# Kernel optimization log

Measured on AMD Instinct MI355X. Metric: run time of the kernel, lower is better.

## Reference

```python
import jax, jax.numpy as jnp
import numpy as np

B, G, D, H, KD = 32, 512, 128, 4, 32  # batch, graph, embed_dim, n_heads, key_dim=embed//heads
NORM = 1.0 / np.sqrt(KD).astype(np.float32)  # MultiHeadCompat norm_factor = 1/sqrt(key_dim)


def _uniform(k, shape, fan):
    s = 1.0 / np.sqrt(fan).astype(np.float32)
    return jax.random.uniform(k, shape, jnp.float32, -s, s)


def setup_inputs() -> dict:
    key = jax.random.key(0)
    ks = jax.random.split(key, 16)
    inp = {
        "h": jax.random.normal(ks[0], (B, G, D), jnp.float32),
        "pos_pickup": jax.random.randint(ks[1], (B,), 0, G),
        "pos_delivery": jax.random.randint(ks[2], (B,), 0, G),
        "rec": jax.random.randint(ks[3], (B, G), 0, G),
        # compater_insert1 / compater_insert2 projections: (n_heads, input_dim, key_dim)
        "Wq1": _uniform(ks[4], (H, D, KD), KD),
        "Wk1": _uniform(ks[5], (H, D, KD), KD),
        "Wq2": _uniform(ks[6], (H, D, KD), KD),
        "Wk2": _uniform(ks[7], (H, D, KD), KD),
        # agg MLP(16, 32, 32, 1); stored as (in, out) so y = x @ W + b
        "fc1_w": _uniform(ks[8], (16, 32), 16),
        "fc1_b": _uniform(ks[9], (32,), 32),
        "fc2_w": _uniform(ks[10], (32, 32), 32),
        "fc2_b": _uniform(ks[11], (32,), 32),
        "fc3_w": _uniform(ks[12], (32, 1), 32),
        "fc3_b": _uniform(ks[13], (1,), 1),
    }
    return inp


def _compat(qv, hh, Wq, Wk):
    # qv: (B, D) single query node; hh: (B, G, D)
    Q = jnp.einsum('bd,hdk->bhk', qv, Wq)       # (B, H, K)
    K = jnp.einsum('bgd,hdk->bhgk', hh, Wk)     # (B, H, G, K)
    return NORM * jnp.einsum('bhk,bhgk->bgh', Q, K)  # (B, G, H)


def reference(h, pos_pickup, pos_delivery, rec, Wq1, Wk1, Wq2, Wk2,
              fc1_w, fc1_b, fc2_w, fc2_b, fc3_w, fc3_b):
    b, g, d = h.shape
    ar = jnp.arange(b)
    h_pickup = h[ar, pos_pickup]      # (B, D)
    h_delivery = h[ar, pos_delivery]  # (B, D)
    h_neighbour = jnp.take_along_axis(h, rec[:, :, None], axis=1)  # (B, G, D)

    shp = (b, g, g, 4)
    c_pp = jnp.broadcast_to(_compat(h_pickup, h, Wq1, Wk1)[:, :, None, :], shp)
    c_po = jnp.broadcast_to(_compat(h_pickup, h_neighbour, Wq2, Wk2)[:, :, None, :], shp)
    c_dp = jnp.broadcast_to(_compat(h_delivery, h, Wq1, Wk1)[:, None, :, :], shp)
    c_do = jnp.broadcast_to(_compat(h_delivery, h_neighbour, Wq2, Wk2)[:, None, :, :], shp)
    x = jnp.concatenate([c_pp, c_po, c_dp, c_do], axis=-1)  # (B, G, G, 16)

    # agg MLP (dropout p=0.05 is identity at inference)
    x = jax.nn.relu(x @ fc1_w + fc1_b)
    x = jax.nn.relu(x @ fc2_w + fc2_b)
    return (x @ fc3_w + fc3_b)[..., 0]  # (B, G, G)
```

## Files before the change

kernel.cpp:

```cpp
#include <hip/hip_runtime.h>


#define B 32
#define G 512
#define D 128
#define NH 4
#define KD 32
#define NORMF 0.17677669529663687f

#define WS_P16H 131072
#define WS_Q16H 655360

typedef float v16f __attribute__((ext_vector_type(16)));
typedef _Float16 v8h __attribute__((ext_vector_type(8)));
typedef _Float16 h2v __attribute__((ext_vector_type(2)));

struct HQ { h2v h[4]; };

__device__ __forceinline__ v8h relu_add(const HQ& p, const HQ& q) {
  const h2v z = {(_Float16)0.0f, (_Float16)0.0f};
  HQ r;
#pragma unroll
  for (int i = 0; i < 4; ++i)
    r.h[i] = __builtin_elementwise_max(p.h[i] + q.h[i], z);
  return __builtin_bit_cast(v8h, r);
}

__global__ __launch_bounds__(256) void stage01(
    const float* __restrict__ h, const int* __restrict__ pp,
    const int* __restrict__ pd, const int* __restrict__ rec,
    const float* __restrict__ Wq1, const float* __restrict__ Wk1,
    const float* __restrict__ Wq2, const float* __restrict__ Wk2,
    const float* __restrict__ fc1_w, const float* __restrict__ fc1_b,
    float* __restrict__ ws) {
  const int bx = blockIdx.x;
  const int b = bx >> 3, g0 = (bx & 7) * 64;
  const int t = threadIdx.x;

  __shared__ float hp[D], hd[D];
  __shared__ float qq[4][NH * KD];
  __shared__ float sA[4][NH][D];
  __shared__ float sc[64][17];
  __shared__ float sout[64][33];

  if (t < 128) {
    hp[t] = h[((size_t)b * G + pp[b]) * D + t];
  } else {
    const int u = t - 128;
    hd[u] = h[((size_t)b * G + pd[b]) * D + u];
  }
  __syncthreads();

  if (t < 128) {
    const int hh = t >> 5, k = t & 31;
    const float* wq1 = Wq1 + hh * D * KD + k;
    const float* wq2 = Wq2 + hh * D * KD + k;
    float s1p = 0.f, s2p = 0.f, s1d = 0.f, s2d = 0.f;
    for (int d = 0; d < D; ++d) {
      const float w1 = wq1[d * KD], w2 = wq2[d * KD];
      const float xp = hp[d], xd = hd[d];
      s1p = fmaf(xp, w1, s1p);
      s2p = fmaf(xp, w2, s2p);
      s1d = fmaf(xd, w1, s1d);
      s2d = fmaf(xd, w2, s2d);
    }
    qq[0][t] = s1p; qq[1][t] = s2p; qq[2][t] = s1d; qq[3][t] = s2d;
  }
  __syncthreads();

  {
    const int d = t & 127;
    const int h0 = (t >> 7) * 2;
#pragma unroll
    for (int hh = h0; hh < h0 + 2; ++hh) {
      const float* wk1 = Wk1 + hh * D * KD + d * KD;
      const float* wk2 = Wk2 + hh * D * KD + d * KD;
      float apq = 0.f, apo = 0.f, adp = 0.f, ado = 0.f;
#pragma unroll
      for (int k = 0; k < KD; ++k) {
        const float w1 = wk1[k], w2 = wk2[k];
        apq = fmaf(qq[0][hh * 32 + k], w1, apq);
        adp = fmaf(qq[2][hh * 32 + k], w1, adp);
        apo = fmaf(qq[1][hh * 32 + k], w2, apo);
        ado = fmaf(qq[3][hh * 32 + k], w2, ado);
      }
      sA[0][hh][d] = NORMF * apq;
      sA[1][hh][d] = NORMF * apo;
      sA[2][hh][d] = NORMF * adp;
      sA[3][hh][d] = NORMF * ado;
    }
  }
  __syncthreads();

  const int gl = t & 63;
  const int hh = __builtin_amdgcn_readfirstlane(t >> 6);
  const int g = g0 + gl;
  const float4* hg4 = (const float4*)(h + ((size_t)b * G + g) * D);
  const float4* hn4 = (const float4*)(h + ((size_t)b * G + rec[b * G + g]) * D);

  float cpp = 0.f, cpo = 0.f, cdp = 0.f, cdo = 0.f;
#pragma unroll 4
  for (int d4 = 0; d4 < 32; ++d4) {
    const float4 x = hg4[d4], y = hn4[d4];
    const float4 a1 = *(const float4*)&sA[0][hh][4 * d4];
    const float4 a2 = *(const float4*)&sA[1][hh][4 * d4];
    const float4 a3 = *(const float4*)&sA[2][hh][4 * d4];
    const float4 a4 = *(const float4*)&sA[3][hh][4 * d4];
    cpp = fmaf(x.x, a1.x, fmaf(x.y, a1.y, fmaf(x.z, a1.z, fmaf(x.w, a1.w, cpp))));
    cpo = fmaf(y.x, a2.x, fmaf(y.y, a2.y, fmaf(y.z, a2.z, fmaf(y.w, a2.w, cpo))));
    cdp = fmaf(x.x, a3.x, fmaf(x.y, a3.y, fmaf(x.z, a3.z, fmaf(x.w, a3.w, cdp))));
    cdo = fmaf(y.x, a4.x, fmaf(y.y, a4.y, fmaf(y.z, a4.z, fmaf(y.w, a4.w, cdo))));
  }
  sc[gl][hh] = cpp; sc[gl][4 + hh] = cpo; sc[gl][8 + hh] = cdp; sc[gl][12 + hh] = cdo;
  __syncthreads();

  float u[16];
#pragma unroll
  for (int i = 0; i < 16; ++i) u[i] = sc[gl][i];

  float pv[8], qv[8];
#pragma unroll
  for (int jj = 0; jj < 8; ++jj) {
    const int j = hh * 8 + jj;
    float p = 0.f, q = fc1_b[j];
#pragma unroll
    for (int i = 0; i < 8; ++i) {
      p = fmaf(u[i], fc1_w[i * 32 + j], p);
      q = fmaf(u[8 + i], fc1_w[(8 + i) * 32 + j], q);
    }
    pv[jj] = p; qv[jj] = q;
  }

#pragma unroll
  for (int jj = 0; jj < 8; ++jj) sout[gl][hh * 8 + jj] = pv[jj];
  __syncthreads();
  {
    unsigned* dst = (unsigned*)((unsigned short*)ws + WS_P16H) +
                    ((size_t)b * G + g0) * 16;
#pragma unroll
    for (int i = t; i < 1024; i += 256) {
      const int row = i >> 4, c0 = (2 * i) & 31;
      __fp16 __attribute__((ext_vector_type(2))) pk =
          __builtin_amdgcn_cvt_pkrtz(sout[row][c0], sout[row][c0 + 1]);
      dst[i] = *(const unsigned*)&pk;
    }
  }
  __syncthreads();
#pragma unroll
  for (int jj = 0; jj < 8; ++jj) sout[gl][hh * 8 + jj] = qv[jj];
  __syncthreads();
  {
    unsigned* dst = (unsigned*)((unsigned short*)ws + WS_Q16H) +
                    ((size_t)b * G + g0) * 16;
#pragma unroll
    for (int i = t; i < 1024; i += 256) {
      const int row = i >> 4, c0 = (2 * i) & 31;
      __fp16 __attribute__((ext_vector_type(2))) pk =
          __builtin_amdgcn_cvt_pkrtz(sout[row][c0], sout[row][c0 + 1]);
      dst[i] = *(const unsigned*)&pk;
    }
  }
}

__global__ __launch_bounds__(256) void mlp_pairs(
    const float* __restrict__ ws,
    const float* __restrict__ fc2_w, const float* __restrict__ fc2_b,
    const float* __restrict__ fc3_w, const float* __restrict__ fc3_b,
    float* __restrict__ out) {
  const int b = blockIdx.z;
  const int g1_0 = blockIdx.y * 16;
  const int g2_0 = blockIdx.x * 128;
  const int t = threadIdx.x;
  const int w = t >> 6, l = t & 63;
  const int col = l & 31;
  const int half = l >> 5;
  const int kb = half * 8;

  __shared__ __align__(16) unsigned short sPh[16 * 32];
  {
    const unsigned* Psrc = (const unsigned*)((const unsigned short*)ws + WS_P16H) +
                           ((size_t)b * G + g1_0) * 16;
    ((unsigned*)sPh)[t] = Psrc[t];
  }

  v8h A0, A1;
#pragma unroll
  for (int j = 0; j < 8; ++j) {
    A0[j] = (_Float16)fc2_w[(kb + j) * 32 + col];
    A1[j] = (_Float16)fc2_w[(16 + kb + j) * 32 + col];
  }
  v16f biasC;
  float w3v[16];
#pragma unroll
  for (int r = 0; r < 16; ++r) {
    const int n = (r & 3) + 8 * (r >> 2) + 4 * half;
    biasC[r] = fc2_b[n];
    w3v[r]   = fc3_w[n];
  }
  const float b3 = fc3_b[0];

  HQ qlo, qhi;
  {
    const unsigned short* qp = (const unsigned short*)ws + WS_Q16H +
        ((size_t)b * G + g2_0 + w * 32 + col) * 32;
    qlo = __builtin_bit_cast(HQ, *(const uint4*)(qp + kb));
    qhi = __builtin_bit_cast(HQ, *(const uint4*)(qp + 16 + kb));
  }
  __syncthreads();

  float* op = out + (((size_t)b * G + g1_0 + half) * G) + g2_0 + w * 32 + col;
#pragma unroll
  for (int i = 0; i < 8; ++i) {
    const int ra = 2 * i, rb = 2 * i + 1;
    const HQ palo = __builtin_bit_cast(HQ, *(const uint4*)(sPh + ra * 32 + kb));
    const HQ pahi = __builtin_bit_cast(HQ, *(const uint4*)(sPh + ra * 32 + 16 + kb));
    const HQ pblo = __builtin_bit_cast(HQ, *(const uint4*)(sPh + rb * 32 + kb));
    const HQ pbhi = __builtin_bit_cast(HQ, *(const uint4*)(sPh + rb * 32 + 16 + kb));

    const v8h Balo = relu_add(palo, qlo);
    const v8h Bahi = relu_add(pahi, qhi);
    const v8h Bblo = relu_add(pblo, qlo);
    const v8h Bbhi = relu_add(pbhi, qhi);

    v16f acca = __builtin_amdgcn_mfma_f32_32x32x16_f16(A0, Balo, biasC, 0, 0, 0);
    v16f accb = __builtin_amdgcn_mfma_f32_32x32x16_f16(A0, Bblo, biasC, 0, 0, 0);
    acca = __builtin_amdgcn_mfma_f32_32x32x16_f16(A1, Bahi, acca, 0, 0, 0);
    accb = __builtin_amdgcn_mfma_f32_32x32x16_f16(A1, Bbhi, accb, 0, 0, 0);

    float a0 = 0.f, a1 = 0.f, b0 = 0.f, b1 = 0.f;
#pragma unroll
    for (int r = 0; r < 16; r += 2) {
      a0 = fmaf(fmaxf(acca[r], 0.f), w3v[r], a0);
      a1 = fmaf(fmaxf(acca[r + 1], 0.f), w3v[r + 1], a1);
      b0 = fmaf(fmaxf(accb[r], 0.f), w3v[r], b0);
      b1 = fmaf(fmaxf(accb[r + 1], 0.f), w3v[r + 1], b1);
    }
    float sa = a0 + a1, sb = b0 + b1;
    sa += __shfl_xor(sa, 32);
    sb += __shfl_xor(sb, 32);
    op[(size_t)ra * G] = (half ? sb : sa) + b3;
  }
}

extern "C" void kernel_launch(void* const* d_in, const int* in_sizes, int n_in,
                              void* d_out, int out_size, void* d_ws, size_t ws_size,
                              hipStream_t stream) {
  const float* h     = (const float*)d_in[0];
  const int*   pp    = (const int*)d_in[1];
  const int*   pd    = (const int*)d_in[2];
  const int*   rec   = (const int*)d_in[3];
  const float* Wq1   = (const float*)d_in[4];
  const float* Wk1   = (const float*)d_in[5];
  const float* Wq2   = (const float*)d_in[6];
  const float* Wk2   = (const float*)d_in[7];
  const float* fc1_w = (const float*)d_in[8];
  const float* fc1_b = (const float*)d_in[9];
  const float* fc2_w = (const float*)d_in[10];
  const float* fc2_b = (const float*)d_in[11];
  const float* fc3_w = (const float*)d_in[12];
  const float* fc3_b = (const float*)d_in[13];
  float* out = (float*)d_out;
  float* ws  = (float*)d_ws;

  stage01<<<dim3(256), dim3(256), 0, stream>>>(
      h, pp, pd, rec, Wq1, Wk1, Wq2, Wk2, fc1_w, fc1_b, ws);
  mlp_pairs<<<dim3(4, 32, 32), dim3(256), 0, stream>>>(
      ws, fc2_w, fc2_b, fc3_w, fc3_b, out);
}
```

Baseline: 148.9 us.

## Double g2 tile per block, reuse P rows across two Q columns, pack epilogue

Each wave now covers two 32-wide g2 column groups against all 16 g1 rows, where before it covered one group against row pairs. Each P row loaded from shared memory feeds two MFMA chains, and the grid shrinks by half in x. The layer-3 epilogue uses packed float2 max/fma, and a single cross-half shuffle replaces two. The aim is fewer LDS reads, fewer shuffles and less VALU per output, at the cost of more registers per thread and fewer blocks.

```diff
diff --git a/kernel.cpp b/kernel.cpp
--- a/kernel.cpp
+++ b/kernel.cpp
@@ -12,10 +12,12 @@
 #define WS_Q16H 655360
 
 typedef float v16f __attribute__((ext_vector_type(16)));
+typedef float f2v __attribute__((ext_vector_type(2)));
 typedef _Float16 v8h __attribute__((ext_vector_type(8)));
 typedef _Float16 h2v __attribute__((ext_vector_type(2)));
 
 struct HQ { h2v h[4]; };
+struct F2x8 { f2v v[8]; };
 
 __device__ __forceinline__ v8h relu_add(const HQ& p, const HQ& q) {
   const h2v z = {(_Float16)0.0f, (_Float16)0.0f};
@@ -169,7 +171,7 @@
     float* __restrict__ out) {
   const int b = blockIdx.z;
   const int g1_0 = blockIdx.y * 16;
-  const int g2_0 = blockIdx.x * 128;
+  const int g2_0 = blockIdx.x * 256;
   const int t = threadIdx.x;
   const int w = t >> 6, l = t & 63;
   const int col = l & 31;
@@ -190,55 +192,57 @@
     A1[j] = (_Float16)fc2_w[(16 + kb + j) * 32 + col];
   }
   v16f biasC;
-  float w3v[16];
+  F2x8 w3p;
 #pragma unroll
   for (int r = 0; r < 16; ++r) {
     const int n = (r & 3) + 8 * (r >> 2) + 4 * half;
     biasC[r] = fc2_b[n];
-    w3v[r]   = fc3_w[n];
+    ((float*)&w3p)[r] = fc3_w[n];
   }
   const float b3 = fc3_b[0];
 
-  HQ qlo, qhi;
-  {
+  HQ qlo[2], qhi[2];
+#pragma unroll
+  for (int c = 0; c < 2; ++c) {
     const unsigned short* qp = (const unsigned short*)ws + WS_Q16H +
-        ((size_t)b * G + g2_0 + w * 32 + col) * 32;
-    qlo = __builtin_bit_cast(HQ, *(const uint4*)(qp + kb));
-    qhi = __builtin_bit_cast(HQ, *(const uint4*)(qp + 16 + kb));
-  }
-  __syncthreads();
-
-  float* op = out + (((size_t)b * G + g1_0 + half) * G) + g2_0 + w * 32 + col;
-#pragma unroll
-  for (int i = 0; i < 8; ++i) {
-    const int ra = 2 * i, rb = 2 * i + 1;
-    const HQ palo = __builtin_bit_cast(HQ, *(const uint4*)(sPh + ra * 32 + kb));
-    const HQ pahi = __builtin_bit_cast(HQ, *(const uint4*)(sPh + ra * 32 + 16 + kb));
-    const HQ pblo = __builtin_bit_cast(HQ, *(const uint4*)(sPh + rb * 32 + kb));
-    const HQ pbhi = __builtin_bit_cast(HQ, *(const uint4*)(sPh + rb * 32 + 16 + kb));
-
-    const v8h Balo = relu_add(palo, qlo);
-    const v8h Bahi = relu_add(pahi, qhi);
-    const v8h Bblo = relu_add(pblo, qlo);
-    const v8h Bbhi = relu_add(pbhi, qhi);
-
-    v16f acca = __builtin_amdgcn_mfma_f32_32x32x16_f16(A0, Balo, biasC, 0, 0, 0);
-    v16f accb = __builtin_amdgcn_mfma_f32_32x32x16_f16(A0, Bblo, biasC, 0, 0, 0);
-    acca = __builtin_amdgcn_mfma_f32_32x32x16_f16(A1, Bahi, acca, 0, 0, 0);
-    accb = __builtin_amdgcn_mfma_f32_32x32x16_f16(A1, Bbhi, accb, 0, 0, 0);
-
-    float a0 = 0.f, a1 = 0.f, b0 = 0.f, b1 = 0.f;
-#pragma unroll
-    for (int r = 0; r < 16; r += 2) {
-      a0 = fmaf(fmaxf(acca[r], 0.f), w3v[r], a0);
-      a1 = fmaf(fmaxf(acca[r + 1], 0.f), w3v[r + 1], a1);
-      b0 = fmaf(fmaxf(accb[r], 0.f), w3v[r], b0);
-      b1 = fmaf(fmaxf(accb[r + 1], 0.f), w3v[r + 1], b1);
-    }
-    float sa = a0 + a1, sb = b0 + b1;
-    sa += __shfl_xor(sa, 32);
-    sb += __shfl_xor(sb, 32);
-    op[(size_t)ra * G] = (half ? sb : sa) + b3;
+        ((size_t)b * G + g2_0 + (2 * w + c) * 32 + col) * 32;
+    qlo[c] = __builtin_bit_cast(HQ, *(const uint4*)(qp + kb));
+    qhi[c] = __builtin_bit_cast(HQ, *(const uint4*)(qp + 16 + kb));
+  }
+  __syncthreads();
+
+  const f2v z2 = {0.f, 0.f};
+  float* op = out + (((size_t)b * G + g1_0) * G) + g2_0 + w * 64 + half * 32 + col;
+#pragma unroll
+  for (int g1 = 0; g1 < 16; ++g1) {
+    const HQ plo = __builtin_bit_cast(HQ, *(const uint4*)(sPh + g1 * 32 + kb));
+    const HQ phi = __builtin_bit_cast(HQ, *(const uint4*)(sPh + g1 * 32 + 16 + kb));
+
+    const v8h B0lo = relu_add(plo, qlo[0]);
+    const v8h B0hi = relu_add(phi, qhi[0]);
+    const v8h B1lo = relu_add(plo, qlo[1]);
+    const v8h B1hi = relu_add(phi, qhi[1]);
+
+    v16f acc0 = __builtin_amdgcn_mfma_f32_32x32x16_f16(A0, B0lo, biasC, 0, 0, 0);
+    v16f acc1 = __builtin_amdgcn_mfma_f32_32x32x16_f16(A0, B1lo, biasC, 0, 0, 0);
+    acc0 = __builtin_amdgcn_mfma_f32_32x32x16_f16(A1, B0hi, acc0, 0, 0, 0);
+    acc1 = __builtin_amdgcn_mfma_f32_32x32x16_f16(A1, B1hi, acc1, 0, 0, 0);
+
+    const F2x8 f0 = __builtin_bit_cast(F2x8, acc0);
+    const F2x8 f1 = __builtin_bit_cast(F2x8, acc1);
+    f2v e0 = z2, e1 = z2;
+#pragma unroll
+    for (int i = 0; i < 8; ++i) {
+      e0 = __builtin_elementwise_max(f0.v[i], z2) * w3p.v[i] + e0;
+      e1 = __builtin_elementwise_max(f1.v[i], z2) * w3p.v[i] + e1;
+    }
+    const float sa = e0[0] + e0[1];
+    const float sb = e1[0] + e1[1];
+
+    float y = half ? sb : sa;
+    float zsw = half ? sa : sb;
+    y += __shfl_xor(zsw, 32);
+    op[(size_t)g1 * G] = y + b3;
   }
 }
 
@@ -264,6 +268,6 @@
 
   stage01<<<dim3(256), dim3(256), 0, stream>>>(
       h, pp, pd, rec, Wq1, Wk1, Wq2, Wk2, fc1_w, fc1_b, ws);
-  mlp_pairs<<<dim3(4, 32, 32), dim3(256), 0, stream>>>(
+  mlp_pairs<<<dim3(2, 32, 32), dim3(256), 0, stream>>>(
       ws, fc2_w, fc2_b, fc3_w, fc3_b, out);
 }
```

New measurement: 151.5 us. About the same (+1.7%).
